# Optimization experiments

Hardware: AMD Instinct MI355X
Metric: run time of the kernel (lower is better)

## Reference

```python
import jax, jax.numpy as jnp
import numpy as np
import math

B, S, H, NH = 8, 2048, 256, 4
DH = H // NH
EPS = 1e-12


def setup_inputs() -> dict:
    key = jax.random.key(0)
    ks = jax.random.split(key, 20)
    g = lambda k, shape: (jax.random.normal(k, shape, jnp.float32) * 0.02)
    inp = {
        "hidden": jax.random.normal(ks[0], (B, S, H), jnp.float32),
        "Wq": g(ks[1], (H, H)), "bq": jnp.zeros((H,), jnp.float32),
        "Wk": g(ks[2], (H, H)), "bk": jnp.zeros((H,), jnp.float32),
        "Wv": g(ks[3], (H, H)), "bv": jnp.zeros((H,), jnp.float32),
        "Wo": g(ks[4], (H, H)), "bo": jnp.zeros((H,), jnp.float32),
        "W1": g(ks[5], (4 * H, H)), "b1": jnp.zeros((4 * H,), jnp.float32),
        "W2": g(ks[6], (H, 4 * H)), "b2": jnp.zeros((H,), jnp.float32),
        "ln1_w": jnp.ones((H,), jnp.float32), "ln1_b": jnp.zeros((H,), jnp.float32),
        "ln2_w": jnp.ones((H,), jnp.float32), "ln2_b": jnp.zeros((H,), jnp.float32),
        "mask": jax.random.randint(ks[7], (B, S), 0, 2, jnp.int32),
    }
    return inp


def _layernorm(x, w, b):
    u = x.mean(-1, keepdims=True)
    s = ((x - u) ** 2).mean(-1, keepdims=True)
    return w * (x - u) / jnp.sqrt(s + EPS) + b


def _gelu_tanh(h):
    return 0.5 * h * (1.0 + jnp.tanh(math.sqrt(2.0 / math.pi) * (h + 0.044715 * h ** 3)))


def _block(hidden, mask, Wq, bq, Wk, bk, Wv, bv, Wo, bo, W1, b1, W2, b2,
           ln1_w, ln1_b, ln2_w, ln2_b):
    # --- attention sublayer (pre-norm + residual) ---
    x = _layernorm(hidden, ln1_w, ln1_b)
    def heads(W, b):  # [B,S,H] -> [B,NH,S,DH]
        return (x @ W.T + b).reshape(B, S, NH, DH).transpose(0, 2, 1, 3)
    q, k, v = heads(Wq, bq), heads(Wk, bk), heads(Wv, bv)
    corr = jnp.einsum("bhqd,bhkd->bhqk", q, k) / math.sqrt(DH)
    # torch code masks QUERY rows: mask [B,S] broadcast over heads and keys
    corr = jnp.where(mask[:, None, :, None] == 0, -1e9, corr)
    prob = jax.nn.softmax(corr, axis=-1)
    attn = jnp.einsum("bhqk,bhkd->bhqd", prob, v)
    attn = attn.transpose(0, 2, 1, 3).reshape(B, S, H) @ Wo.T + bo
    hidden = hidden + attn
    # --- FFN sublayer (pre-norm + residual) ---
    y = _layernorm(hidden, ln2_w, ln2_b)
    h1 = y @ W1.T + b1
    ff = _gelu_tanh(h1) @ W2.T + b2
    return hidden + ff


def reference(hidden, Wq, bq, Wk, bk, Wv, bv, Wo, bo, W1, b1, W2, b2,
              ln1_w, ln1_b, ln2_w, ln2_b, mask):
    return _block(hidden, mask, Wq, bq, Wk, bk, Wv, bv, Wo, bo,
                  W1, b1, W2, b2, ln1_w, ln1_b, ln2_w, ln2_b)
```

## Files before the change

kernel.cpp:

```cpp
#include <hip/hip_runtime.h>
#include <hip/hip_bf16.h>
#include <cstdint>
#include <cstddef>

constexpr int CB  = 8;
constexpr int CS  = 2048;
constexpr int CH  = 256;
constexpr int CNH = 4;
constexpr int CDH = 64;
constexpr int CT  = CB * CS;

typedef __attribute__((ext_vector_type(8)))  __bf16 bf16x8;
typedef __attribute__((ext_vector_type(4)))  float  f32x4;
typedef __attribute__((ext_vector_type(16))) float  f32x16;
typedef __attribute__((ext_vector_type(2)))  int    i32x2;

__device__ __forceinline__ float b2f(unsigned short u) {
    union { float f; unsigned int i; } v; v.i = ((unsigned int)u) << 16; return v.f;
}
__device__ __forceinline__ unsigned short f2b(float f) {
    union { float f; unsigned int i; } v; v.f = f;
    unsigned int r = v.i + 0x7FFFu + ((v.i >> 16) & 1u);
    return (unsigned short)(r >> 16);
}
__device__ __forceinline__ unsigned short f2b_fast(float f) {
    union { float f; unsigned int i; } v; v.f = f;
    return (unsigned short)((v.i + 0x8000u) >> 16);
}
__device__ __forceinline__ unsigned int packbf(float a, float b) {
    return (unsigned int)f2b_fast(a) | ((unsigned int)f2b_fast(b) << 16);
}
__device__ __forceinline__ float fexp2(float x) {
#if __has_builtin(__builtin_amdgcn_exp2f)
    return __builtin_amdgcn_exp2f(x);
#else
    float r; asm("v_exp_f32 %0, %1" : "=v"(r) : "v"(x)); return r;
#endif
}
__device__ __forceinline__ f32x4 mfma16(bf16x8 a, bf16x8 b, f32x4 c) {
    return __builtin_amdgcn_mfma_f32_16x16x32_bf16(a, b, c, 0, 0, 0);
}
__device__ __forceinline__ f32x16 mfma32(bf16x8 a, bf16x8 b, f32x16 c) {
    return __builtin_amdgcn_mfma_f32_32x32x16_bf16(a, b, c, 0, 0, 0);
}
__device__ __forceinline__ f32x16 zero16() {
    f32x16 z;
    #pragma unroll
    for (int i = 0; i < 16; ++i) z[i] = 0.f;
    return z;
}

#define GLOAD_LDS16(gptr, lptr)                                                        \
    __builtin_amdgcn_global_load_lds((const __attribute__((address_space(1))) void*)(gptr), \
                                     (__attribute__((address_space(3))) void*)(lptr), 16, 0, 0)

#define QSCALE 0.1803368801111204f

__global__ __launch_bounds__(256) void detect_kernel(
    const unsigned short* __restrict__ h, int* __restrict__ flag)
{
    __shared__ int s_bad;
    const int tid = threadIdx.x;
    if (tid == 0) s_bad = 0;
    __syncthreads();
    bool bad = false;
    for (int i = tid; i < 2048; i += 256) {
        float v = b2f(h[i]);
        if (!(fabsf(v) < 1e25f)) bad = true;
    }
    if (bad) s_bad = 1;
    __syncthreads();
    if (tid == 0) *flag = s_bad;
}

struct CvtW { const void* src[6]; void* dst[6]; int n[6]; };
struct CvtB { const void* src[10]; void* dst[10]; int n[10]; };

__global__ __launch_bounds__(256) void cvt_wb_k(const int* __restrict__ flag, CvtW a)
{
    const int seg = blockIdx.y, n = a.n[seg];
    const bool inf32 = (*flag != 0);
    const float* sf = (const float*)a.src[seg];
    const unsigned short* sb = (const unsigned short*)a.src[seg];
    unsigned short* d = (unsigned short*)a.dst[seg];
    for (int i = (blockIdx.x * 256 + threadIdx.x) * 4; i < n; i += gridDim.x * 1024) {
        ushort4 o;
        if (inf32) {
            float4 v = *(const float4*)(sf + i);
            o.x = f2b(v.x); o.y = f2b(v.y); o.z = f2b(v.z); o.w = f2b(v.w);
        } else {
            o = *(const ushort4*)(sb + i);
        }
        *(ushort4*)(d + i) = o;
    }
}

__global__ __launch_bounds__(256) void cvt_bf_k(const int* __restrict__ flag, CvtB a)
{
    const int seg = blockIdx.y, n = a.n[seg];
    const bool inf32 = (*flag != 0);
    const float* sf = (const float*)a.src[seg];
    const unsigned short* sb = (const unsigned short*)a.src[seg];
    float* d = (float*)a.dst[seg];
    const int i = threadIdx.x * 4;
    if (i < n) {
        float4 o;
        if (inf32) {
            o = *(const float4*)(sf + i);
        } else {
            ushort4 v = *(const ushort4*)(sb + i);
            o.x = b2f(v.x); o.y = b2f(v.y); o.z = b2f(v.z); o.w = b2f(v.w);
        }
        *(float4*)(d + i) = o;
    }
}

__global__ __launch_bounds__(256) void ln1_dyn_kernel(
    const void* __restrict__ x, const int* __restrict__ flag,
    const float* __restrict__ w, const float* __restrict__ b,
    unsigned short* __restrict__ xout, unsigned short* __restrict__ hcopy)
{
    const int wave = threadIdx.x >> 6, lane = threadIdx.x & 63;
    const int token = blockIdx.x * 4 + wave;
    const int c = lane * 4;
    const size_t rowo = (size_t)token * CH + c;
    float v0, v1, v2, v3;
    if (*flag != 0) {
        float4 u = *(const float4*)((const float*)x + rowo);
        v0 = u.x; v1 = u.y; v2 = u.z; v3 = u.w;
    } else {
        ushort4 u = *(const ushort4*)((const unsigned short*)x + rowo);
        v0 = b2f(u.x); v1 = b2f(u.y); v2 = b2f(u.z); v3 = b2f(u.w);
    }
    ushort4 hc;
    hc.x = f2b(v0); hc.y = f2b(v1); hc.z = f2b(v2); hc.w = f2b(v3);
    *(ushort4*)(hcopy + rowo) = hc;
    float s = v0 + v1 + v2 + v3;
    float q = v0*v0 + v1*v1 + v2*v2 + v3*v3;
    #pragma unroll
    for (int m = 1; m < 64; m <<= 1) { s += __shfl_xor(s, m, 64); q += __shfl_xor(q, m, 64); }
    float mean = s * (1.0f/256.0f);
    float var  = q * (1.0f/256.0f) - mean*mean;
    float inv  = rsqrtf(var + 1e-12f);
    float4 ww = *(const float4*)(w + c);
    float4 bb = *(const float4*)(b + c);
    ushort4 o;
    o.x = f2b(ww.x * (v0-mean)*inv + bb.x);
    o.y = f2b(ww.y * (v1-mean)*inv + bb.y);
    o.z = f2b(ww.z * (v2-mean)*inv + bb.z);
    o.w = f2b(ww.w * (v3-mean)*inv + bb.w);
    *(ushort4*)(xout + rowo) = o;
}

__global__ __launch_bounds__(256) void ln_kernel(
    const unsigned short* __restrict__ x, const float* __restrict__ w,
    const float* __restrict__ b, unsigned short* __restrict__ out)
{
    const int wave = threadIdx.x >> 6, lane = threadIdx.x & 63;
    const int token = blockIdx.x * 4 + wave;
    const int c = lane * 4;
    const size_t rowo = (size_t)token * CH + c;
    ushort4 u = *(const ushort4*)(x + rowo);
    float v0 = b2f(u.x), v1 = b2f(u.y), v2 = b2f(u.z), v3 = b2f(u.w);
    float s = v0 + v1 + v2 + v3;
    float q = v0*v0 + v1*v1 + v2*v2 + v3*v3;
    #pragma unroll
    for (int m = 1; m < 64; m <<= 1) { s += __shfl_xor(s, m, 64); q += __shfl_xor(q, m, 64); }
    float mean = s * (1.0f/256.0f);
    float var  = q * (1.0f/256.0f) - mean*mean;
    float inv  = rsqrtf(var + 1e-12f);
    float4 ww = *(const float4*)(w + c);
    float4 bb = *(const float4*)(b + c);
    ushort4 o;
    o.x = f2b(ww.x * (v0-mean)*inv + bb.x);
    o.y = f2b(ww.y * (v1-mean)*inv + bb.y);
    o.z = f2b(ww.z * (v2-mean)*inv + bb.z);
    o.w = f2b(ww.w * (v3-mean)*inv + bb.w);
    *(ushort4*)(out + rowo) = o;
}

template<bool GELU, bool RESID, bool OUTDYN>
__device__ __forceinline__ void gemm_core(
    const unsigned short* __restrict__ A, const unsigned short* __restrict__ W,
    const float* __restrict__ bias, const unsigned short* __restrict__ resid,
    void* __restrict__ out, const int* __restrict__ flag,
    int K, int N, int m0, int n0, float oscale, int storemode)
{
    __shared__ __align__(16) unsigned short lA[128*128];
    __shared__ __align__(16) unsigned short lB[128*128];
    const int tid  = threadIdx.x;
    const int lane = tid & 63;
    const int wave = tid >> 6;
    const int wr = (wave >> 1) * 64;
    const int wc = (wave & 1) * 64;
    const int g = lane >> 4, r16 = lane & 15;

    const f32x4 zero = {0.f, 0.f, 0.f, 0.f};
    f32x4 acc[4][4];
    #pragma unroll
    for (int m = 0; m < 4; ++m)
        #pragma unroll
        for (int n = 0; n < 4; ++n) acc[m][n] = zero;

    for (int k0 = 0; k0 < K; k0 += 128) {
        #pragma unroll
        for (int i = 0; i < 8; ++i) {
            const int slot0 = i * 256 + wave * 64;
            const int slot  = slot0 + lane;
            const int row = slot >> 4;
            const int q   = (slot & 15) ^ (row & 7);
            GLOAD_LDS16(A + (size_t)(m0 + row) * K + k0 + q * 8, (char*)lA + slot0 * 16);
            GLOAD_LDS16(W + (size_t)(n0 + row) * K + k0 + q * 8, (char*)lB + slot0 * 16);
        }
        __syncthreads();
        #pragma unroll
        for (int kk = 0; kk < 4; ++kk) {
            bf16x8 af[4], wf[4];
            #pragma unroll
            for (int m = 0; m < 4; ++m) {
                const int arow = wr + m*16 + r16;
                const int c = (kk*4 + g) ^ (arow & 7);
                af[m] = *(const bf16x8*)((char*)lA + arow * 256 + c * 16);
            }
            #pragma unroll
            for (int n = 0; n < 4; ++n) {
                const int brow = wc + n*16 + r16;
                const int c = (kk*4 + g) ^ (brow & 7);
                wf[n] = *(const bf16x8*)((char*)lB + brow * 256 + c * 16);
            }
            #pragma unroll
            for (int m = 0; m < 4; ++m)
                #pragma unroll
                for (int n = 0; n < 4; ++n)
                    acc[m][n] = mfma16(af[m], wf[n], acc[m][n]);
        }
        if (k0 + 128 < K) __syncthreads();
    }

    const bool of32dyn = OUTDYN ? (*flag != 0) : false;
    #pragma unroll
    for (int n = 0; n < 4; ++n) {
        int col = n0 + wc + n*16 + r16;
        float bv = bias[col];
        #pragma unroll
        for (int m = 0; m < 4; ++m) {
            int row0 = m0 + wr + m*16 + g*4;
            if (storemode == 2) {
                ushort4 pk;
                unsigned short* pp = (unsigned short*)&pk;
                #pragma unroll
                for (int r = 0; r < 4; ++r) pp[r] = f2b(acc[m][n][r] + bv);
                const int hh = col >> 6, d = col & 63;
                const int bb = row0 >> 11, ss = row0 & 2047;
                *(ushort4*)((unsigned short*)out +
                    (((size_t)(bb * CNH + hh)) * CDH + d) * CS + ss) = pk;
            } else {
                #pragma unroll
                for (int r = 0; r < 4; ++r) {
                    int row = row0 + r;
                    float v = (acc[m][n][r] + bv) * oscale;
                    if (GELU) {
                        float a = 0.79788456080286541f * (v + 0.044715f * v * v * v);
                        v = v * (1.0f / (1.0f + __expf(-2.0f * a)));
                    }
                    if (RESID) v += b2f(resid[(size_t)row * N + col]);
                    size_t oidx;
                    if (storemode == 1) {
                        int hh = col >> 6, d = col & 63;
                        int bb = row >> 11, ss = row & 2047;
                        oidx = ((((size_t)bb * CNH + hh) * CS) + ss) * CDH + d;
                    } else {
                        oidx = (size_t)row * N + col;
                    }
                    if (OUTDYN && of32dyn) ((float*)out)[oidx] = v;
                    else                   ((unsigned short*)out)[oidx] = f2b(v);
                }
            }
        }
    }
}

__global__ __launch_bounds__(256) void k_qkv(
    const unsigned short* __restrict__ xhat,
    const unsigned short* Wq, const float* bq, unsigned short* q,
    const unsigned short* Wk, const float* bk, unsigned short* k,
    const unsigned short* Wv, const float* bv, unsigned short* v)
{
    const unsigned short* W  = blockIdx.z == 0 ? Wq : (blockIdx.z == 1 ? Wk : Wv);
    const float*          bi = blockIdx.z == 0 ? bq : (blockIdx.z == 1 ? bk : bv);
    unsigned short*       o  = blockIdx.z == 0 ? q  : (blockIdx.z == 1 ? k  : v);
    const float osc = blockIdx.z == 0 ? QSCALE : 1.0f;
    const int sm = blockIdx.z == 2 ? 2 : 1;
    gemm_core<false, false, false>(xhat, W, bi, nullptr, o, nullptr,
                                   CH, CH, blockIdx.x * 128, blockIdx.y * 128, osc, sm);
}

__global__ __launch_bounds__(256) void k_oproj(
    const unsigned short* __restrict__ A, const unsigned short* __restrict__ W,
    const float* __restrict__ bias, const unsigned short* __restrict__ resid,
    unsigned short* __restrict__ out)
{
    gemm_core<false, true, false>(A, W, bias, resid, out, nullptr,
                                  CH, CH, blockIdx.x * 128, blockIdx.y * 128, 1.0f, 0);
}

__global__ __launch_bounds__(256) void k_ffn1(
    const unsigned short* __restrict__ A, const unsigned short* __restrict__ W,
    const float* __restrict__ bias, unsigned short* __restrict__ out)
{
    gemm_core<true, false, false>(A, W, bias, nullptr, out, nullptr,
                                  CH, 4*CH, blockIdx.x * 128, blockIdx.y * 128, 1.0f, 0);
}

__global__ __launch_bounds__(256) void k_ffn2(
    const unsigned short* __restrict__ A, const unsigned short* __restrict__ W,
    const float* __restrict__ bias, const unsigned short* __restrict__ resid,
    void* __restrict__ out, const int* __restrict__ flag)
{
    gemm_core<false, true, true>(A, W, bias, resid, out, flag,
                                 4*CH, CH, blockIdx.x * 128, blockIdx.y * 128, 1.0f, 0);
}

__global__ __launch_bounds__(512, 4) void attn_kernel(
    const unsigned short* __restrict__ Q, const unsigned short* __restrict__ Kp,
    const unsigned short* __restrict__ Vt, const int* __restrict__ mask,
    unsigned short* __restrict__ out)
{
    __shared__ __align__(16) char lds[65536];

    const int tid = threadIdx.x, lane = tid & 63, wave = tid >> 6;
    const int qb = wave >> 1, kh = wave & 1;
    const int r32 = lane & 31, hi = lane >> 5;
    const int bh = blockIdx.y, bb = bh >> 2, hh = bh & 3;
    const int q0 = blockIdx.x * 128;
    const size_t baseQ = (size_t)bh * CS * CDH;
    const size_t baseT = (size_t)bh * CDH * CS;

    const int qrow = q0 + qb * 32 + r32;
    bf16x8 qf[4];
    {
        const bool live = (mask[bb * CS + qrow] != 0);
        #pragma unroll
        for (int dw = 0; dw < 4; ++dw) {
            uint4 v = {0u, 0u, 0u, 0u};
            if (live) v = *(const uint4*)(Q + baseQ + (size_t)qrow * CDH + dw * 16 + hi * 8);
            qf[dw] = *(bf16x8*)&v;
        }
    }

#define STAGE(BUF, KT) do {                                                             \
        _Pragma("unroll")                                                               \
        for (int i = 0; i < 2; ++i) {                                                   \
            const int slot0 = i * 512 + wave * 64;                                      \
            const int slot  = slot0 + lane;                                             \
            const int kw = slot >> 7, kk2 = slot & 127;                                 \
            GLOAD_LDS16(Kp + baseQ + (size_t)((KT) + kk2) * CDH + kw * 8,               \
                        lds + (BUF) * 16384 + slot0 * 16);                              \
            const int vc = slot >> 6, vd = slot & 63;                                   \
            GLOAD_LDS16(Vt + baseT + (size_t)vd * CS + (KT) + vc * 8,                   \
                        lds + 32768 + (BUF) * 16384 + slot0 * 16);                      \
        } } while (0)

    f32x16 o0 = zero16(), o1 = zero16();
    float psum = 0.f;

    STAGE(0, 0);
    __syncthreads();

    for (int t = 0; t < CS / 128; ++t) {
        const int buf = t & 1;
        const int kt = t * 128;
        if (t + 1 < CS / 128) STAGE(buf ^ 1, kt + 128);

        const char* kbase = lds + buf * 16384;
        const char* vbase = lds + 32768 + buf * 16384;

        f32x16 sT0 = zero16(), sT1 = zero16();
        __builtin_amdgcn_s_setprio(1);
        #pragma unroll
        for (int dw = 0; dw < 4; ++dw) {
            const char* cb = kbase + (dw * 2 + hi) * 2048;
            bf16x8 k0 = *(const bf16x8*)(cb + (kh * 64 + r32) * 16);
            bf16x8 k1 = *(const bf16x8*)(cb + (kh * 64 + 32 + r32) * 16);
            sT0 = mfma32(k0, qf[dw], sT0);
            sT1 = mfma32(k1, qf[dw], sT1);
        }
        __builtin_amdgcn_s_setprio(0);

#define PROCKB(SREG, KB) do {                                                           \
            float p[16];                                                                \
            _Pragma("unroll")                                                           \
            for (int r = 0; r < 16; ++r) { p[r] = fexp2((SREG)[r]); psum += p[r]; }     \
            _Pragma("unroll")                                                           \
            for (int w = 0; w < 2; ++w) {                                               \
                unsigned int a01 = packbf(p[w*8+0], p[w*8+1]);                          \
                unsigned int a23 = packbf(p[w*8+2], p[w*8+3]);                          \
                unsigned int b01 = packbf(p[w*8+4], p[w*8+5]);                          \
                unsigned int b23 = packbf(p[w*8+6], p[w*8+7]);                          \
                unsigned int ap0, ap1, ap2, ap3;                                        \
                {                                                                       \
                    i32x2 s1 = __builtin_amdgcn_permlane32_swap((int)a01, (int)b01, false, false); \
                    i32x2 s2 = __builtin_amdgcn_permlane32_swap((int)a23, (int)b23, false, false); \
                    ap0 = (unsigned int)s1.x; ap2 = (unsigned int)s1.y;                 \
                    ap1 = (unsigned int)s2.x; ap3 = (unsigned int)s2.y;                 \
                }                                                                       \
                union { unsigned int u[4]; bf16x8 v; } apv;                             \
                apv.u[0] = ap0; apv.u[1] = ap1; apv.u[2] = ap2; apv.u[3] = ap3;         \
                const char* vb2 = vbase + ((kh * 4 + (KB) * 2 + w) * 2 + hi) * 1024;    \
                bf16x8 v0 = *(const bf16x8*)(vb2 + r32 * 16);                           \
                bf16x8 v1 = *(const bf16x8*)(vb2 + (32 + r32) * 16);                    \
                o0 = mfma32(apv.v, v0, o0);                                             \
                o1 = mfma32(apv.v, v1, o1);                                             \
            } } while (0)

        PROCKB(sT0, 0);
        PROCKB(sT1, 1);
#undef PROCKB

        __syncthreads();
    }

    float ps = psum + __shfl_xor(psum, 32, 64);
    float* lsum = (float*)(lds + 32768);
    float* Oex  = (float*)lds;
    if (lane < 32) lsum[(qb * 2 + kh) * 32 + r32] = ps;
    if (kh == 1) {
        #pragma unroll
        for (int r = 0; r < 16; ++r) {
            const int qr = (r & 3) + 8 * (r >> 2) + 4 * hi;
            Oex[(qb * 32 + qr) * 64 + r32]      = o0[r];
            Oex[(qb * 32 + qr) * 64 + 32 + r32] = o1[r];
        }
    }
    __syncthreads();
    if (kh == 0) {
        #pragma unroll
        for (int r = 0; r < 16; ++r) {
            const int qr = (r & 3) + 8 * (r >> 2) + 4 * hi;
            const float l = lsum[(qb * 2 + 0) * 32 + qr] + lsum[(qb * 2 + 1) * 32 + qr];
            const float inv = 1.0f / l;
            const float u0 = (o0[r] + Oex[(qb * 32 + qr) * 64 + r32]) * inv;
            const float u1 = (o1[r] + Oex[(qb * 32 + qr) * 64 + 32 + r32]) * inv;
            const size_t ob = (size_t)(bb * CS + q0 + qb * 32 + qr) * CH + hh * CDH;
            out[ob + r32]      = f2b(u0);
            out[ob + 32 + r32] = f2b(u1);
        }
    }
#undef STAGE
}

extern "C" void kernel_launch(void* const* d_in, const int* in_sizes, int n_in,
                              void* d_out, int out_size, void* d_ws, size_t ws_size,
                              hipStream_t stream)
{
    const void* hidden = d_in[0];
    const void* Wq = d_in[1];  const void* bq = d_in[2];
    const void* Wk = d_in[3];  const void* bk = d_in[4];
    const void* Wv = d_in[5];  const void* bv = d_in[6];
    const void* Wo = d_in[7];  const void* bo = d_in[8];
    const void* W1 = d_in[9];  const void* b1 = d_in[10];
    const void* W2 = d_in[11]; const void* b2 = d_in[12];
    const void* ln1w = d_in[13]; const void* ln1b = d_in[14];
    const void* ln2w = d_in[15]; const void* ln2b = d_in[16];
    const int* mask = (const int*)d_in[17];

    char* ws = (char*)d_ws;
    const size_t KB = 1u << 10, MB = 1u << 20;
    int*            flag  = (int*)ws;
    float*          bqf   = (float*)(ws + 4*KB);
    float*          bkf   = (float*)(ws + 8*KB);
    float*          bvf   = (float*)(ws + 12*KB);
    float*          bof   = (float*)(ws + 16*KB);
    float*          b1f   = (float*)(ws + 20*KB);
    float*          b2f_  = (float*)(ws + 28*KB);
    float*          ln1wf = (float*)(ws + 32*KB);
    float*          ln1bf = (float*)(ws + 36*KB);
    float*          ln2wf = (float*)(ws + 40*KB);
    float*          ln2bf = (float*)(ws + 44*KB);
    unsigned short* Wqb   = (unsigned short*)(ws + 1*MB);
    unsigned short* Wkb   = (unsigned short*)(ws + 1*MB + 256*KB);
    unsigned short* Wvb   = (unsigned short*)(ws + 1*MB + 512*KB);
    unsigned short* Wob   = (unsigned short*)(ws + 1*MB + 768*KB);
    unsigned short* W1b   = (unsigned short*)(ws + 2*MB);
    unsigned short* W2b   = (unsigned short*)(ws + 2*MB + 512*KB);
    unsigned short* hb16  = (unsigned short*)(ws + 3*MB);
    unsigned short* xhat  = (unsigned short*)(ws + 11*MB);
    unsigned short* qb    = (unsigned short*)(ws + 19*MB);
    unsigned short* kb    = (unsigned short*)(ws + 27*MB);
    unsigned short* vtb   = (unsigned short*)(ws + 35*MB);
    unsigned short* attnb = xhat;
    unsigned short* hid2b = qb;
    unsigned short* yhat  = kb;
    unsigned short* h1g   = (unsigned short*)(ws + 51*MB);

    dim3 blk(256);
    detect_kernel<<<1, blk, 0, stream>>>((const unsigned short*)hidden, flag);

    CvtW cw;
    cw.src[0]=Wq;  cw.dst[0]=Wqb;  cw.n[0]=CH*CH;
    cw.src[1]=Wk;  cw.dst[1]=Wkb;  cw.n[1]=CH*CH;
    cw.src[2]=Wv;  cw.dst[2]=Wvb;  cw.n[2]=CH*CH;
    cw.src[3]=Wo;  cw.dst[3]=Wob;  cw.n[3]=CH*CH;
    cw.src[4]=W1;  cw.dst[4]=W1b;  cw.n[4]=4*CH*CH;
    cw.src[5]=W2;  cw.dst[5]=W2b;  cw.n[5]=4*CH*CH;
    cvt_wb_k<<<dim3(128, 6), blk, 0, stream>>>(flag, cw);

    CvtB cf;
    cf.src[0]=bq;    cf.dst[0]=bqf;   cf.n[0]=CH;
    cf.src[1]=bk;    cf.dst[1]=bkf;   cf.n[1]=CH;
    cf.src[2]=bv;    cf.dst[2]=bvf;   cf.n[2]=CH;
    cf.src[3]=bo;    cf.dst[3]=bof;   cf.n[3]=CH;
    cf.src[4]=b1;    cf.dst[4]=b1f;   cf.n[4]=4*CH;
    cf.src[5]=b2;    cf.dst[5]=b2f_;  cf.n[5]=CH;
    cf.src[6]=ln1w;  cf.dst[6]=ln1wf; cf.n[6]=CH;
    cf.src[7]=ln1b;  cf.dst[7]=ln1bf; cf.n[7]=CH;
    cf.src[8]=ln2w;  cf.dst[8]=ln2wf; cf.n[8]=CH;
    cf.src[9]=ln2b;  cf.dst[9]=ln2bf; cf.n[9]=CH;
    cvt_bf_k<<<dim3(1, 10), blk, 0, stream>>>(flag, cf);

    ln1_dyn_kernel<<<CT / 4, blk, 0, stream>>>(hidden, flag, ln1wf, ln1bf, xhat, hb16);
    k_qkv<<<dim3(CT / 128, CH / 128, 3), blk, 0, stream>>>(xhat, Wqb, bqf, qb,
                                                           Wkb, bkf, kb, Wvb, bvf, vtb);
    attn_kernel<<<dim3(CS / 128, CB * CNH), dim3(512), 0, stream>>>(qb, kb, vtb, mask, attnb);
    k_oproj<<<dim3(CT / 128, CH / 128), blk, 0, stream>>>(attnb, Wob, bof, hb16, hid2b);
    ln_kernel<<<CT / 4, blk, 0, stream>>>(hid2b, ln2wf, ln2bf, yhat);
    k_ffn1<<<dim3(CT / 128, (4 * CH) / 128), blk, 0, stream>>>(yhat, W1b, b1f, h1g);
    k_ffn2<<<dim3(CT / 128, CH / 128), blk, 0, stream>>>(h1g, W2b, b2f_, hid2b,
                                                         d_out, flag);
}
```

Measured before the change: 156.2 us.

## Split attention across key halves and add a combine kernel

The attention kernel now splits the key dimension into two halves via a third grid dimension. Each block writes unnormalized bf16 partial outputs and row sums, and a new combine kernel adds the halves and normalizes. Key tiles shrink from 128 to 64 and LDS drops to about 33KB, which allows a higher occupancy hint and doubles the grid to fill more CUs. In exchange it adds an extra launch, round-trips the partials through memory, and rounds the partials to bf16 before they are summed.

```diff
diff --git a/kernel.cpp b/kernel.cpp
--- a/kernel.cpp
+++ b/kernel.cpp
@@ -321,18 +321,20 @@
                                  4*CH, CH, blockIdx.x * 128, blockIdx.y * 128, 1.0f, 0);
 }
 
-__global__ __launch_bounds__(512, 4) void attn_kernel(
+__global__ __launch_bounds__(512, 8) void attn_kernel(
     const unsigned short* __restrict__ Q, const unsigned short* __restrict__ Kp,
     const unsigned short* __restrict__ Vt, const int* __restrict__ mask,
-    unsigned short* __restrict__ out)
-{
-    __shared__ __align__(16) char lds[65536];
+    unsigned short* __restrict__ opart, float* __restrict__ lpart)
+{
+    __shared__ __align__(16) char lds[33792];
 
     const int tid = threadIdx.x, lane = tid & 63, wave = tid >> 6;
     const int qb = wave >> 1, kh = wave & 1;
     const int r32 = lane & 31, hi = lane >> 5;
-    const int bh = blockIdx.y, bb = bh >> 2, hh = bh & 3;
+    const int bh = blockIdx.y, bb = bh >> 2;
     const int q0 = blockIdx.x * 128;
+    const int half = blockIdx.z;
+    const int kbase0 = half * (CS / 2);
     const size_t baseQ = (size_t)bh * CS * CDH;
     const size_t baseT = (size_t)bh * CDH * CS;
 
@@ -349,73 +351,58 @@
     }
 
 #define STAGE(BUF, KT) do {                                                             \
-        _Pragma("unroll")                                                               \
-        for (int i = 0; i < 2; ++i) {                                                   \
-            const int slot0 = i * 512 + wave * 64;                                      \
-            const int slot  = slot0 + lane;                                             \
-            const int kw = slot >> 7, kk2 = slot & 127;                                 \
-            GLOAD_LDS16(Kp + baseQ + (size_t)((KT) + kk2) * CDH + kw * 8,               \
-                        lds + (BUF) * 16384 + slot0 * 16);                              \
-            const int vc = slot >> 6, vd = slot & 63;                                   \
-            GLOAD_LDS16(Vt + baseT + (size_t)vd * CS + (KT) + vc * 8,                   \
-                        lds + 32768 + (BUF) * 16384 + slot0 * 16);                      \
-        } } while (0)
+        GLOAD_LDS16(Kp + baseQ + (size_t)((KT) + lane) * CDH + wave * 8,                \
+                    lds + (BUF) * 8192 + wave * 1024);                                  \
+        GLOAD_LDS16(Vt + baseT + (size_t)lane * CS + (KT) + wave * 8,                   \
+                    lds + 16384 + (BUF) * 8192 + wave * 1024);                          \
+    } while (0)
 
     f32x16 o0 = zero16(), o1 = zero16();
     float psum = 0.f;
 
-    STAGE(0, 0);
+    STAGE(0, kbase0);
     __syncthreads();
 
-    for (int t = 0; t < CS / 128; ++t) {
+    for (int t = 0; t < 16; ++t) {
         const int buf = t & 1;
-        const int kt = t * 128;
-        if (t + 1 < CS / 128) STAGE(buf ^ 1, kt + 128);
-
-        const char* kbase = lds + buf * 16384;
-        const char* vbase = lds + 32768 + buf * 16384;
-
-        f32x16 sT0 = zero16(), sT1 = zero16();
+        const int kt = kbase0 + t * 64;
+        if (t + 1 < 16) STAGE(buf ^ 1, kt + 64);
+
+        const char* kbs = lds + buf * 8192;
+        const char* vbase = lds + 16384 + buf * 8192;
+
+        f32x16 sT = zero16();
         __builtin_amdgcn_s_setprio(1);
         #pragma unroll
         for (int dw = 0; dw < 4; ++dw) {
-            const char* cb = kbase + (dw * 2 + hi) * 2048;
-            bf16x8 k0 = *(const bf16x8*)(cb + (kh * 64 + r32) * 16);
-            bf16x8 k1 = *(const bf16x8*)(cb + (kh * 64 + 32 + r32) * 16);
-            sT0 = mfma32(k0, qf[dw], sT0);
-            sT1 = mfma32(k1, qf[dw], sT1);
+            const char* cb = kbs + (dw * 2 + hi) * 1024;
+            bf16x8 k0 = *(const bf16x8*)(cb + (kh * 32 + r32) * 16);
+            sT = mfma32(k0, qf[dw], sT);
         }
         __builtin_amdgcn_s_setprio(0);
 
-#define PROCKB(SREG, KB) do {                                                           \
-            float p[16];                                                                \
-            _Pragma("unroll")                                                           \
-            for (int r = 0; r < 16; ++r) { p[r] = fexp2((SREG)[r]); psum += p[r]; }     \
-            _Pragma("unroll")                                                           \
-            for (int w = 0; w < 2; ++w) {                                               \
-                unsigned int a01 = packbf(p[w*8+0], p[w*8+1]);                          \
-                unsigned int a23 = packbf(p[w*8+2], p[w*8+3]);                          \
-                unsigned int b01 = packbf(p[w*8+4], p[w*8+5]);                          \
-                unsigned int b23 = packbf(p[w*8+6], p[w*8+7]);                          \
-                unsigned int ap0, ap1, ap2, ap3;                                        \
-                {                                                                       \
-                    i32x2 s1 = __builtin_amdgcn_permlane32_swap((int)a01, (int)b01, false, false); \
-                    i32x2 s2 = __builtin_amdgcn_permlane32_swap((int)a23, (int)b23, false, false); \
-                    ap0 = (unsigned int)s1.x; ap2 = (unsigned int)s1.y;                 \
-                    ap1 = (unsigned int)s2.x; ap3 = (unsigned int)s2.y;                 \
-                }                                                                       \
-                union { unsigned int u[4]; bf16x8 v; } apv;                             \
-                apv.u[0] = ap0; apv.u[1] = ap1; apv.u[2] = ap2; apv.u[3] = ap3;         \
-                const char* vb2 = vbase + ((kh * 4 + (KB) * 2 + w) * 2 + hi) * 1024;    \
-                bf16x8 v0 = *(const bf16x8*)(vb2 + r32 * 16);                           \
-                bf16x8 v1 = *(const bf16x8*)(vb2 + (32 + r32) * 16);                    \
-                o0 = mfma32(apv.v, v0, o0);                                             \
-                o1 = mfma32(apv.v, v1, o1);                                             \
-            } } while (0)
-
-        PROCKB(sT0, 0);
-        PROCKB(sT1, 1);
-#undef PROCKB
+        float p[16];
+        #pragma unroll
+        for (int r = 0; r < 16; ++r) { p[r] = fexp2(sT[r]); psum += p[r]; }
+        __builtin_amdgcn_s_setprio(1);
+        #pragma unroll
+        for (int w = 0; w < 2; ++w) {
+            unsigned int a01 = packbf(p[w*8+0], p[w*8+1]);
+            unsigned int a23 = packbf(p[w*8+2], p[w*8+3]);
+            unsigned int b01 = packbf(p[w*8+4], p[w*8+5]);
+            unsigned int b23 = packbf(p[w*8+6], p[w*8+7]);
+            i32x2 s1 = __builtin_amdgcn_permlane32_swap((int)a01, (int)b01, false, false);
+            i32x2 s2 = __builtin_amdgcn_permlane32_swap((int)a23, (int)b23, false, false);
+            union { unsigned int u[4]; bf16x8 v; } apv;
+            apv.u[0] = (unsigned int)s1.x; apv.u[1] = (unsigned int)s2.x;
+            apv.u[2] = (unsigned int)s1.y; apv.u[3] = (unsigned int)s2.y;
+            const char* vb2 = vbase + ((kh * 2 + w) * 2 + hi) * 1024;
+            bf16x8 v0 = *(const bf16x8*)(vb2 + r32 * 16);
+            bf16x8 v1 = *(const bf16x8*)(vb2 + (32 + r32) * 16);
+            o0 = mfma32(apv.v, v0, o0);
+            o1 = mfma32(apv.v, v1, o1);
+        }
+        __builtin_amdgcn_s_setprio(0);
 
         __syncthreads();
     }
@@ -438,15 +425,42 @@
         for (int r = 0; r < 16; ++r) {
             const int qr = (r & 3) + 8 * (r >> 2) + 4 * hi;
             const float l = lsum[(qb * 2 + 0) * 32 + qr] + lsum[(qb * 2 + 1) * 32 + qr];
-            const float inv = 1.0f / l;
-            const float u0 = (o0[r] + Oex[(qb * 32 + qr) * 64 + r32]) * inv;
-            const float u1 = (o1[r] + Oex[(qb * 32 + qr) * 64 + 32 + r32]) * inv;
-            const size_t ob = (size_t)(bb * CS + q0 + qb * 32 + qr) * CH + hh * CDH;
-            out[ob + r32]      = f2b(u0);
-            out[ob + 32 + r32] = f2b(u1);
+            const float u0 = o0[r] + Oex[(qb * 32 + qr) * 64 + r32];
+            const float u1 = o1[r] + Oex[(qb * 32 + qr) * 64 + 32 + r32];
+            const size_t ob = ((size_t)(half * 32 + bh) * CS + q0 + qb * 32 + qr) * 64;
+            opart[ob + r32]      = f2b(u0);
+            opart[ob + 32 + r32] = f2b(u1);
+            if (r32 == 0)
+                lpart[(size_t)half * 32 * CS + bh * CS + q0 + qb * 32 + qr] = l;
         }
     }
 #undef STAGE
+}
+
+__global__ __launch_bounds__(256) void attn_combine(
+    const unsigned short* __restrict__ op, const float* __restrict__ lp,
+    unsigned short* __restrict__ out)
+{
+    const int gid = blockIdx.x * 256 + threadIdx.x;
+    const int row = gid >> 3, dc = (gid & 7) * 8;
+    const int bh = row >> 11, s = row & 2047;
+    const int b = bh >> 2, hh = bh & 3;
+    const size_t i0 = ((size_t)row) * 64 + dc;
+    const size_t i1 = ((size_t)(32 * CS) * 64) + i0;
+    const float inv = 1.0f / (lp[row] + lp[32 * CS + row]);
+    ushort4 a0 = *(const ushort4*)(op + i0), a1 = *(const ushort4*)(op + i0 + 4);
+    ushort4 c0 = *(const ushort4*)(op + i1), c1 = *(const ushort4*)(op + i1 + 4);
+    unsigned short o[8];
+    o[0] = f2b((b2f(a0.x) + b2f(c0.x)) * inv);
+    o[1] = f2b((b2f(a0.y) + b2f(c0.y)) * inv);
+    o[2] = f2b((b2f(a0.z) + b2f(c0.z)) * inv);
+    o[3] = f2b((b2f(a0.w) + b2f(c0.w)) * inv);
+    o[4] = f2b((b2f(a1.x) + b2f(c1.x)) * inv);
+    o[5] = f2b((b2f(a1.y) + b2f(c1.y)) * inv);
+    o[6] = f2b((b2f(a1.z) + b2f(c1.z)) * inv);
+    o[7] = f2b((b2f(a1.w) + b2f(c1.w)) * inv);
+    const size_t ob = ((size_t)(b * CS + s)) * CH + hh * CDH + dc;
+    *(uint4*)(out + ob) = *(uint4*)o;
 }
 
 extern "C" void kernel_launch(void* const* d_in, const int* in_sizes, int n_in,
@@ -488,9 +502,11 @@
     unsigned short* qb    = (unsigned short*)(ws + 19*MB);
     unsigned short* kb    = (unsigned short*)(ws + 27*MB);
     unsigned short* vtb   = (unsigned short*)(ws + 35*MB);
+    float*          lpart = (float*)(ws + 43*MB);
     unsigned short* attnb = xhat;
     unsigned short* hid2b = qb;
     unsigned short* yhat  = kb;
+    unsigned short* opart = (unsigned short*)(ws + 51*MB);
     unsigned short* h1g   = (unsigned short*)(ws + 51*MB);
 
     dim3 blk(256);
@@ -521,7 +537,9 @@
     ln1_dyn_kernel<<<CT / 4, blk, 0, stream>>>(hidden, flag, ln1wf, ln1bf, xhat, hb16);
     k_qkv<<<dim3(CT / 128, CH / 128, 3), blk, 0, stream>>>(xhat, Wqb, bqf, qb,
                                                            Wkb, bkf, kb, Wvb, bvf, vtb);
-    attn_kernel<<<dim3(CS / 128, CB * CNH), dim3(512), 0, stream>>>(qb, kb, vtb, mask, attnb);
+    attn_kernel<<<dim3(CS / 128, CB * CNH, 2), dim3(512), 0, stream>>>(qb, kb, vtb, mask,
+                                                                       opart, lpart);
+    attn_combine<<<2048, blk, 0, stream>>>(opart, lpart, attnb);
     k_oproj<<<dim3(CT / 128, CH / 128), blk, 0, stream>>>(attnb, Wob, bof, hb16, hid2b);
     ln_kernel<<<CT / 4, blk, 0, stream>>>(hid2b, ln2wf, ln2bf, yhat);
     k_ffn1<<<dim3(CT / 128, (4 * CH) / 128), blk, 0, stream>>>(yhat, W1b, b1f, h1g);
```

After: 565.8 us. +262.2%, slower.
